# Kernel tuning notes

Measured on AMD Instinct MI355X. Metric: run time of the kernel, lower is better.

The kernel has to match this reference:

```python
import jax, jax.numpy as jnp
import numpy as np

NUM_NODES = 8192
NUM_EDGES = 262144
IN_C = 512
OUT_C = 512


def setup_inputs() -> dict:
    key = jax.random.key(0)
    k1, k2, k3, k4 = jax.random.split(key, 4)
    x = jax.random.normal(k1, (NUM_NODES, IN_C), dtype=jnp.float32)
    edge_index = jax.random.randint(k2, (2, NUM_EDGES), 0, NUM_NODES, dtype=jnp.int64)
    # nn.Linear params (W: [out, in], b: [out]) with kaiming-ish scale
    W = jax.random.normal(k3, (OUT_C, IN_C), dtype=jnp.float32) * (1.0 / np.sqrt(IN_C))
    b = jax.random.normal(k4, (OUT_C,), dtype=jnp.float32) * 0.01
    return {"x": x, "edge_index": edge_index, "W": W, "b": b}


def reference(x, edge_index, W, b):
    n = x.shape[0]
    # append self loops
    loop = jnp.arange(n, dtype=edge_index.dtype)
    rows = jnp.concatenate([edge_index[0], loop])
    cols = jnp.concatenate([edge_index[1], loop])
    # dense adjacency via scatter-set (duplicates collapse to 1.0, matching torch indexing assign)
    adj = jnp.zeros((n, n), dtype=jnp.float32).at[rows, cols].set(1.0)
    deg = adj.sum(axis=1)
    deg_inv_sqrt = jnp.where(deg > 0, jax.lax.rsqrt(jnp.maximum(deg, 1e-30)), 0.0)
    norm = deg_inv_sqrt[:, None] * adj * deg_inv_sqrt[None, :]
    h = x @ W.T + b            # [N, out_c]
    return norm @ h            # [N, out_c]
```

## Files before the change

### kernel.cpp

```cpp
#include <hip/hip_runtime.h>
#include <stdint.h>

#define N_NODES 8192
#define N_EDGES 262144
#define IN_C    512
#define OUT_C   512
#define MAX_DEG 128
#define X_ELEMS (N_NODES * IN_C)
#define W_ELEMS (OUT_C * IN_C)
#define BM_WORDS (N_NODES * (N_NODES / 32))

typedef __attribute__((ext_vector_type(8))) short short8;
typedef __attribute__((ext_vector_type(4))) float f32x4;

__device__ inline uint16_t f2bf(float f) {
    uint32_t u = __float_as_uint(f);
    uint32_t r = (u + 0x7FFFu + ((u >> 16) & 1u)) >> 16;
    return (uint16_t)r;
}

#define GLOAD_LDS16(g, l)                                                        \
    __builtin_amdgcn_global_load_lds(                                            \
        (const __attribute__((address_space(1))) uint32_t*)(g),                  \
        (__attribute__((address_space(3))) uint32_t*)(l), 16, 0, 0)

__global__ __launch_bounds__(256) void convert_k(const float* __restrict__ x,
                                                 const float* __restrict__ W,
                                                 uint16_t* __restrict__ xb,
                                                 uint16_t* __restrict__ wb,
                                                 int* __restrict__ cnt,
                                                 uint4* __restrict__ bm) {
    int tid = blockIdx.x * 256 + threadIdx.x;
    if (tid < N_NODES) cnt[tid] = 0;
    if (tid < BM_WORDS / 4) bm[tid] = make_uint4(0u, 0u, 0u, 0u);
    int i = tid * 8;
    const float* src; uint16_t* dst;
    if (i < X_ELEMS) { src = x + i; dst = xb + i; }
    else             { src = W + (i - X_ELEMS); dst = wb + (i - X_ELEMS); }
    float4 v0 = *(const float4*)(src);
    float4 v1 = *(const float4*)(src + 4);
    ushort4 o0, o1;
    o0.x = f2bf(v0.x); o0.y = f2bf(v0.y); o0.z = f2bf(v0.z); o0.w = f2bf(v0.w);
    o1.x = f2bf(v1.x); o1.y = f2bf(v1.y); o1.z = f2bf(v1.z); o1.w = f2bf(v1.w);
    *(ushort4*)(dst)     = o0;
    *(ushort4*)(dst + 4) = o1;
}

__global__ __launch_bounds__(256) void gemm_scatter_k(const uint16_t* __restrict__ xb,
                                                      const uint16_t* __restrict__ wb,
                                                      const float* __restrict__ bias,
                                                      uint16_t* __restrict__ h,
                                                      const int* __restrict__ ei,
                                                      int* __restrict__ cnt,
                                                      uint16_t* __restrict__ nbr,
                                                      uint32_t* __restrict__ bm) {
    __shared__ uint16_t lA[128 * 64];
    __shared__ uint16_t lB[128 * 64];
    const int bid = blockIdx.x;
    if (bid < 256) {
        const int wave = threadIdx.x >> 6;
        const int lane = threadIdx.x & 63;
        const int quad = lane >> 4;
        const int l16  = lane & 15;
        const int mrow = (bid & 7) * 8 + (bid >> 5);
        const int ncol = (bid >> 3) & 3;
        const int m0 = mrow * 128;
        const int n0 = ncol * 128;
        const int wm = wave & 1;
        const int wn = wave >> 1;

        const int srow = wave * 32 + (lane >> 3);
        const int scol = (lane & 7) * 8;
        uint16_t* lAdst = &lA[wave * 32 * 64];
        uint16_t* lBdst = &lB[wave * 32 * 64];

        f32x4 acc[4][4];
        #pragma unroll
        for (int a = 0; a < 4; a++)
            #pragma unroll
            for (int s = 0; s < 4; s++) acc[a][s] = (f32x4){0.f, 0.f, 0.f, 0.f};

        for (int k0 = 0; k0 < IN_C; k0 += 64) {
            #pragma unroll
            for (int it = 0; it < 4; it++) {
                GLOAD_LDS16(xb + (m0 + srow + it * 8) * IN_C + k0 + scol, lAdst + it * 8 * 64);
                GLOAD_LDS16(wb + (n0 + srow + it * 8) * IN_C + k0 + scol, lBdst + it * 8 * 64);
            }
            __syncthreads();
            #pragma unroll
            for (int kk = 0; kk < 2; kk++) {
                short8 af[4], bfr[4];
                #pragma unroll
                for (int a = 0; a < 4; a++)
                    af[a] = *(const short8*)&lA[(wm * 64 + a * 16 + l16) * 64 + kk * 32 + quad * 8];
                #pragma unroll
                for (int s = 0; s < 4; s++)
                    bfr[s] = *(const short8*)&lB[(wn * 64 + s * 16 + l16) * 64 + kk * 32 + quad * 8];
                #pragma unroll
                for (int a = 0; a < 4; a++)
                    #pragma unroll
                    for (int s = 0; s < 4; s++)
                        acc[a][s] = __builtin_amdgcn_mfma_f32_16x16x32_bf16(bfr[s], af[a], acc[a][s], 0, 0, 0);
            }
            __syncthreads();
        }
        const int m_base = m0 + wm * 64;
        const int n_base = n0 + wn * 64;
        #pragma unroll
        for (int s = 0; s < 4; s++) {
            int col_n0 = n_base + s * 16 + quad * 4;
            float4 bv = *(const float4*)(bias + col_n0);
            #pragma unroll
            for (int a = 0; a < 4; a++) {
                int row_m = m_base + a * 16 + l16;
                ushort4 o;
                o.x = f2bf(acc[a][s][0] + bv.x);
                o.y = f2bf(acc[a][s][1] + bv.y);
                o.z = f2bf(acc[a][s][2] + bv.z);
                o.w = f2bf(acc[a][s][3] + bv.w);
                *(ushort4*)(h + row_m * OUT_C + col_n0) = o;
            }
        }
    } else {
        int t = (bid - 256) * 256 + threadIdx.x;
        int r, c;
        if (t < N_EDGES) {
            r = ei[t];
            c = ei[N_EDGES + t];
        } else if (t < N_EDGES + N_NODES) {
            r = t - N_EDGES; c = r;
        } else return;
        uint32_t w   = (uint32_t)r * (uint32_t)(N_NODES / 32) + ((uint32_t)c >> 5);
        uint32_t bit = 1u << (c & 31);
        uint32_t old = atomicOr(&bm[w], bit);
        if (!(old & bit)) {
            int pos = atomicAdd(&cnt[r], 1);
            if (pos < MAX_DEG) nbr[r * MAX_DEG + pos] = (uint16_t)c;
        }
    }
}

__global__ __launch_bounds__(64) void aggregate_k(const int* __restrict__ cnt,
                                                  const uint16_t* __restrict__ nbr,
                                                  const uint32_t* __restrict__ h2,
                                                  float* __restrict__ out) {
    const int i    = blockIdx.x >> 2;
    const int q    = blockIdx.x & 3;
    const int lane = threadIdx.x;
    int m = cnt[i]; if (m > MAX_DEG) m = MAX_DEG;

    __shared__ uint16_t jl[MAX_DEG];
    __shared__ float    dl[MAX_DEG];
    for (int t = lane; t < m; t += 64) {
        uint16_t j = nbr[i * MAX_DEG + t];
        jl[t] = j;
        dl[t] = rsqrtf((float)cnt[j]);
    }
    __syncthreads();

    const uint32_t* hp = h2 + q * 64 + lane;
    float s0 = 0.f, s1 = 0.f;
    #pragma unroll 8
    for (int l = 0; l < m; l++) {
        uint32_t u = hp[(int)jl[l] * 256];
        float dj = dl[l];
        s0 += dj * __uint_as_float(u << 16);
        s1 += dj * __uint_as_float(u & 0xFFFF0000u);
    }
    float di = rsqrtf((float)m);
    int c = q * 128 + lane * 2;
    float2 o = {di * s0, di * s1};
    *(float2*)(out + i * OUT_C + c) = o;
}

extern "C" void kernel_launch(void* const* d_in, const int* in_sizes, int n_in,
                              void* d_out, int out_size, void* d_ws, size_t ws_size,
                              hipStream_t stream) {
    const float* x  = (const float*)d_in[0];
    const int*   ei = (const int*)  d_in[1];
    const float* W  = (const float*)d_in[2];
    const float* b  = (const float*)d_in[3];
    float* out = (float*)d_out;
    char* ws = (char*)d_ws;

    const size_t CNT_OFF = 0;
    const size_t BM_OFF  = 32768;
    const size_t NBR_OFF = BM_OFF + 8388608;
    const size_t XB_OFF  = NBR_OFF + 2097152;
    const size_t WB_OFF  = XB_OFF + 8388608;
    const size_t H_OFF   = WB_OFF + 524288;
    int*      cnt = (int*)     (ws + CNT_OFF);
    uint32_t* bm  = (uint32_t*)(ws + BM_OFF);
    uint16_t* nbr = (uint16_t*)(ws + NBR_OFF);
    uint16_t* xb  = (uint16_t*)(ws + XB_OFF);
    uint16_t* wb  = (uint16_t*)(ws + WB_OFF);
    uint16_t* h   = (uint16_t*)(ws + H_OFF);

    convert_k<<<(X_ELEMS + W_ELEMS) / (256 * 8), 256, 0, stream>>>(x, W, xb, wb, cnt, (uint4*)bm);

    gemm_scatter_k<<<256 + (N_EDGES + N_NODES + 255) / 256, 256, 0, stream>>>(
        xb, wb, b, h, ei, cnt, nbr, bm);

    aggregate_k<<<N_NODES * 4, 64, 0, stream>>>(cnt, nbr, (const uint32_t*)h, out);
}
```

Baseline: 122.5 us.

## Fuse x fp32-to-bf16 conversion into GEMM A-tile loading

Removes the separate bf16 copy of x. The GEMM now reads fp32 x directly through registers, converts it, and writes it to LDS. The convert kernel shrinks to zeroing the bitmap and converting W, with a grid sized by bitmap words. This avoids writing and re-reading an 8 MB intermediate, but the A loads become synchronous register round-trips instead of async global_load_lds, and each GEMM block reads twice the bytes for A.

```diff
diff --git a/kernel.cpp b/kernel.cpp
--- a/kernel.cpp
+++ b/kernel.cpp
@@ -6,7 +6,6 @@
 #define IN_C    512
 #define OUT_C   512
 #define MAX_DEG 128
-#define X_ELEMS (N_NODES * IN_C)
 #define W_ELEMS (OUT_C * IN_C)
 #define BM_WORDS (N_NODES * (N_NODES / 32))
 
@@ -24,29 +23,26 @@
         (const __attribute__((address_space(1))) uint32_t*)(g),                  \
         (__attribute__((address_space(3))) uint32_t*)(l), 16, 0, 0)
 
-__global__ __launch_bounds__(256) void convert_k(const float* __restrict__ x,
-                                                 const float* __restrict__ W,
-                                                 uint16_t* __restrict__ xb,
+__global__ __launch_bounds__(256) void convert_k(const float* __restrict__ W,
                                                  uint16_t* __restrict__ wb,
                                                  int* __restrict__ cnt,
                                                  uint4* __restrict__ bm) {
     int tid = blockIdx.x * 256 + threadIdx.x;
     if (tid < N_NODES) cnt[tid] = 0;
-    if (tid < BM_WORDS / 4) bm[tid] = make_uint4(0u, 0u, 0u, 0u);
-    int i = tid * 8;
-    const float* src; uint16_t* dst;
-    if (i < X_ELEMS) { src = x + i; dst = xb + i; }
-    else             { src = W + (i - X_ELEMS); dst = wb + (i - X_ELEMS); }
-    float4 v0 = *(const float4*)(src);
-    float4 v1 = *(const float4*)(src + 4);
-    ushort4 o0, o1;
-    o0.x = f2bf(v0.x); o0.y = f2bf(v0.y); o0.z = f2bf(v0.z); o0.w = f2bf(v0.w);
-    o1.x = f2bf(v1.x); o1.y = f2bf(v1.y); o1.z = f2bf(v1.z); o1.w = f2bf(v1.w);
-    *(ushort4*)(dst)     = o0;
-    *(ushort4*)(dst + 4) = o1;
-}
-
-__global__ __launch_bounds__(256) void gemm_scatter_k(const uint16_t* __restrict__ xb,
+    bm[tid] = make_uint4(0u, 0u, 0u, 0u);
+    if (tid < W_ELEMS / 8) {
+        int i = tid * 8;
+        float4 v0 = *(const float4*)(W + i);
+        float4 v1 = *(const float4*)(W + i + 4);
+        ushort4 o0, o1;
+        o0.x = f2bf(v0.x); o0.y = f2bf(v0.y); o0.z = f2bf(v0.z); o0.w = f2bf(v0.w);
+        o1.x = f2bf(v1.x); o1.y = f2bf(v1.y); o1.z = f2bf(v1.z); o1.w = f2bf(v1.w);
+        *(ushort4*)(wb + i)     = o0;
+        *(ushort4*)(wb + i + 4) = o1;
+    }
+}
+
+__global__ __launch_bounds__(256) void gemm_scatter_k(const float* __restrict__ x,
                                                       const uint16_t* __restrict__ wb,
                                                       const float* __restrict__ bias,
                                                       uint16_t* __restrict__ h,
@@ -71,8 +67,10 @@
 
         const int srow = wave * 32 + (lane >> 3);
         const int scol = (lane & 7) * 8;
-        uint16_t* lAdst = &lA[wave * 32 * 64];
         uint16_t* lBdst = &lB[wave * 32 * 64];
+
+        const int arow = lane >> 4;
+        const int acol = (lane & 15) * 4;
 
         f32x4 acc[4][4];
         #pragma unroll
@@ -82,9 +80,19 @@
 
         for (int k0 = 0; k0 < IN_C; k0 += 64) {
             #pragma unroll
-            for (int it = 0; it < 4; it++) {
-                GLOAD_LDS16(xb + (m0 + srow + it * 8) * IN_C + k0 + scol, lAdst + it * 8 * 64);
+            for (int it = 0; it < 4; it++)
                 GLOAD_LDS16(wb + (n0 + srow + it * 8) * IN_C + k0 + scol, lBdst + it * 8 * 64);
+            float4 av[8];
+            #pragma unroll
+            for (int rnd = 0; rnd < 8; rnd++)
+                av[rnd] = *(const float4*)(x + (size_t)(m0 + wave * 32 + rnd * 4 + arow) * IN_C
+                                           + k0 + acol);
+            #pragma unroll
+            for (int rnd = 0; rnd < 8; rnd++) {
+                ushort4 o;
+                o.x = f2bf(av[rnd].x); o.y = f2bf(av[rnd].y);
+                o.z = f2bf(av[rnd].z); o.w = f2bf(av[rnd].w);
+                *(ushort4*)&lA[(wave * 32 + rnd * 4 + arow) * 64 + acol] = o;
             }
             __syncthreads();
             #pragma unroll
@@ -186,20 +194,18 @@
     const size_t CNT_OFF = 0;
     const size_t BM_OFF  = 32768;
     const size_t NBR_OFF = BM_OFF + 8388608;
-    const size_t XB_OFF  = NBR_OFF + 2097152;
-    const size_t WB_OFF  = XB_OFF + 8388608;
+    const size_t WB_OFF  = NBR_OFF + 2097152;
     const size_t H_OFF   = WB_OFF + 524288;
     int*      cnt = (int*)     (ws + CNT_OFF);
     uint32_t* bm  = (uint32_t*)(ws + BM_OFF);
     uint16_t* nbr = (uint16_t*)(ws + NBR_OFF);
-    uint16_t* xb  = (uint16_t*)(ws + XB_OFF);
     uint16_t* wb  = (uint16_t*)(ws + WB_OFF);
     uint16_t* h   = (uint16_t*)(ws + H_OFF);
 
-    convert_k<<<(X_ELEMS + W_ELEMS) / (256 * 8), 256, 0, stream>>>(x, W, xb, wb, cnt, (uint4*)bm);
+    convert_k<<<BM_WORDS / 4 / 256, 256, 0, stream>>>(W, wb, cnt, (uint4*)bm);
 
     gemm_scatter_k<<<256 + (N_EDGES + N_NODES + 255) / 256, 256, 0, stream>>>(
-        xb, wb, b, h, ei, cnt, nbr, bm);
+        x, wb, b, h, ei, cnt, nbr, bm);
 
     aggregate_k<<<N_NODES * 4, 64, 0, stream>>>(cnt, nbr, (const uint32_t*)h, out);
 }
```

Result: no change. 120.8 us (median of 2 runs) (-1.4%).
